# Performance work log

Hardware: AMD Instinct MI355X
Metric: run time of the kernel (lower is better)

The kernel has to match this reference:

```python
import jax, jax.numpy as jnp
import numpy as np

N, E = 4096, 131072
D_IN, D_H, H, D_HEAD, D_OUT, L = 768, 256, 4, 64, 128, 2


def setup_inputs() -> dict:
    key = jax.random.key(0)
    ks = jax.random.split(key, 8)
    x = jax.random.normal(ks[0], (N, D_IN), dtype=jnp.float32)
    edge_index = jax.random.randint(ks[1], (2, E), 0, N, dtype=jnp.int64)
    Win = jax.random.normal(ks[2], (D_IN, D_H), dtype=jnp.float32) * 0.02
    bin_ = jnp.zeros((D_H,), dtype=jnp.float32)
    # per-layer, per-head projection weights [L, H, D_H, D_HEAD]
    Wg = jax.random.normal(ks[3], (L, H, D_H, D_HEAD), dtype=jnp.float32) * 0.05
    # per-layer, per-head attention vectors a: [L, H, 2*D_HEAD]
    a = jax.random.normal(ks[4], (L, H, 2 * D_HEAD), dtype=jnp.float32) * 0.05
    Wout = jax.random.normal(ks[5], (D_H, D_OUT), dtype=jnp.float32) * 0.05
    bout = jnp.zeros((D_OUT,), dtype=jnp.float32)
    return {"x": x, "edge_index": edge_index, "Win": Win, "bin_": bin_,
            "Wg": Wg, "a": a, "Wout": Wout, "bout": bout}


def _gat_layer(h, Wl, al, row, col):
    # h: [N, D_H], Wl: [H, D_H, D_HEAD], al: [H, 2*D_HEAD]
    hh = jnp.einsum('ni,hio->hno', h, Wl)          # [H, N, D_HEAD]
    a_src, a_dst = al[:, :D_HEAD], al[:, D_HEAD:]
    s_src = jnp.einsum('hno,ho->hn', hh, a_src)    # [H, N]
    s_dst = jnp.einsum('hno,ho->hn', hh, a_dst)    # [H, N]
    e = jax.nn.leaky_relu(s_src[:, row] + s_dst[:, col], negative_slope=0.2)  # [H, E]
    # dense scatter exactly as the torch module: zeros then assign at (row, col)
    att = jnp.zeros((H, N, N), dtype=h.dtype).at[:, row, col].set(e)
    att = jax.nn.softmax(att, axis=-1)             # dense row softmax (zeros included)
    hp = jnp.einsum('hnm,hmo->hno', att, hh)       # [H, N, D_HEAD]
    return jnp.transpose(hp, (1, 0, 2)).reshape(N, H * D_HEAD)


def reference(x, edge_index, Win, bin_, Wg, a, Wout, bout):
    row, col = edge_index[0], edge_index[1]
    h = jax.nn.relu(x @ Win + bin_)                # input_proj + relu (dropout = eval identity)
    for l in range(L):
        h = jax.nn.relu(_gat_layer(h, Wg[l], a[l], row, col))
    node_embeddings = h @ Wout + bout              # [N, D_OUT]
    return node_embeddings
```

## Files before the change

### kernel.cpp

```cpp
#include <hip/hip_runtime.h>
#include <hip/hip_bf16.h>

#define NNODES 4096
#define NEDGES 131072
#define D_IN   768
#define D_H    256
#define NHEAD  4
#define D_HEAD 64
#define D_OUT  128
#define DEGCAP 192
#define S_SCALE 1048576.0f

typedef __attribute__((ext_vector_type(4))) float f32x4;
typedef __attribute__((ext_vector_type(8))) short bf16x8;
typedef __attribute__((ext_vector_type(8))) unsigned short u16x8;

static __device__ __forceinline__ unsigned short f2bf(float f) {
    __hip_bfloat16 h = __float2bfloat16(f);
    return *reinterpret_cast<unsigned short*>(&h);
}
static __device__ __forceinline__ float bf2f(unsigned short u) {
    return __uint_as_float((unsigned)u << 16);
}

#define OFF_XB     (0u)
#define OFF_H0     (6u<<20)
#define OFF_H1     (8u<<20)
#define OFF_HH     (10u<<20)
#define OFF_SINT   (12u<<20)
#define OFF_SSRC   (OFF_SINT + 4096u)
#define OFF_SDST   (OFF_SSRC + 65536u)
#define OFF_WINT   (OFF_SDST + 65536u)
#define OFF_WGT    (OFF_WINT + 393216u)
#define OFF_WOUTT  (OFF_WGT + 262144u)
#define OFF_BM     (OFF_WOUTT + 65536u)

__global__ __launch_bounds__(256) void k_init(
    const float* __restrict__ Win, const float* __restrict__ Wg,
    const float* __restrict__ Wout, const float* __restrict__ x,
    unsigned short* __restrict__ WinT, unsigned short* __restrict__ WgT,
    unsigned short* __restrict__ WoutT, unsigned short* __restrict__ xb,
    uint4* __restrict__ bm4, unsigned long long* __restrict__ Sint)
{
    __shared__ float tile[32][33];
    const int tid = threadIdx.x, bid = blockIdx.x;
    bm4[bid*256 + tid] = make_uint4(0u,0u,0u,0u);
    if (bid == 0) { Sint[tid] = 0ull; Sint[256 + tid] = 0ull; }

    {
        const float4* x4 = (const float4*)x;
        ushort4* xb4 = (ushort4*)xb;
        for (int i = bid*256 + tid; i < (NNODES*D_IN)/4; i += 512*256) {
            float4 v = x4[i];
            ushort4 o;
            o.x = f2bf(v.x); o.y = f2bf(v.y); o.z = f2bf(v.z); o.w = f2bf(v.w);
            xb4[i] = o;
        }
    }

    if (bid < 352) {
        const float* src; unsigned short* dst; int R, Cc, tr, tc;
        if (bid < 192)      { src = Win;  dst = WinT;  R = 768; Cc = 256; tr = bid >> 3; tc = bid & 7; }
        else if (bid < 320) { int t = bid - 192; int m = t >> 4, s = t & 15;
                              src = Wg + (size_t)m*16384; dst = WgT + (size_t)m*16384;
                              R = 256; Cc = 64; tr = s >> 1; tc = s & 1; }
        else                { int t = bid - 320; src = Wout; dst = WoutT;
                              R = 256; Cc = 128; tr = t >> 2; tc = t & 3; }
        int ci = tid & 31, rq = tid >> 5;
        #pragma unroll
        for (int rr = rq; rr < 32; rr += 8)
            tile[rr][ci] = src[(size_t)(tr*32+rr)*Cc + tc*32 + ci];
        __syncthreads();
        int ri = tid & 31, cq = tid >> 5;
        #pragma unroll
        for (int cc = cq; cc < 32; cc += 8)
            dst[(size_t)(tc*32+cc)*R + tr*32 + ri] = f2bf(tile[ri][cc]);
    }
}

__global__ void edge_bitmap(const int* __restrict__ ei, unsigned* __restrict__ bm)
{
    __shared__ int is64_sh;
    int tid = threadIdx.x;
    if (tid < 64) {
        int v = ei[2*tid + 1];
        unsigned long long ball = __ballot(v == 0);
        if (tid == 0) is64_sh = (ball == ~0ull) ? 1 : 0;
    }
    __syncthreads();
    int is64 = is64_sh;
    int k = blockIdx.x*256 + tid;
    if (k >= NEDGES) return;
    int r = is64 ? ei[2*k]            : ei[k];
    int c = is64 ? ei[2*NEDGES + 2*k] : ei[NEDGES + k];
    r &= (NNODES-1); c &= (NNODES-1);
    atomicOr(&bm[(size_t)r*128 + (c>>5)], 1u << (c & 31));
}

__global__ __launch_bounds__(256) void gemm_mfma(
    const unsigned short* __restrict__ A, const unsigned short* __restrict__ BT,
    const float* __restrict__ bias, float* __restrict__ Cf,
    unsigned short* __restrict__ Cb,
    int N, int K, int relu,
    const float* __restrict__ a_l, float* __restrict__ ssrc,
    float* __restrict__ sdst, unsigned long long* __restrict__ Sint)
{
    __shared__ unsigned short As[32][72];
    __shared__ unsigned short Bs[64][72];
    __shared__ float sredS[4][32], sredD[4][32];
    const int tid = threadIdx.x;
    const int bx = blockIdx.x, by = blockIdx.y;
    const int wc = tid >> 6;
    const int lane = tid & 63;
    const int g = lane >> 4, c = lane & 15;
    const int ar = tid >> 3, ak = (tid & 7) * 8;
    const int bc = tid >> 2, bk = (tid & 3) * 16;
    f32x4 acc0 = {0.f,0.f,0.f,0.f}, acc1 = {0.f,0.f,0.f,0.f};
    const unsigned short* Arow = A + (size_t)(by*32 + ar)*K;
    const unsigned short* Brow = BT + (size_t)(bx*64 + bc)*K;

    for (int k0 = 0; k0 < K; k0 += 64) {
        u16x8 avv = *(const u16x8*)&Arow[k0 + ak];
        u16x8 bv0 = *(const u16x8*)&Brow[k0 + bk];
        u16x8 bv1 = *(const u16x8*)&Brow[k0 + bk + 8];
        *(u16x8*)&As[ar][ak]     = avv;
        *(u16x8*)&Bs[bc][bk]     = bv0;
        *(u16x8*)&Bs[bc][bk + 8] = bv1;
        __syncthreads();
        bf16x8 b0  = *(bf16x8*)&Bs[wc*16 + c][g*8];
        bf16x8 b1  = *(bf16x8*)&Bs[wc*16 + c][32 + g*8];
        bf16x8 a00 = *(bf16x8*)&As[c][g*8];
        bf16x8 a01 = *(bf16x8*)&As[c][32 + g*8];
        bf16x8 a10 = *(bf16x8*)&As[16 + c][g*8];
        bf16x8 a11 = *(bf16x8*)&As[16 + c][32 + g*8];
        acc0 = __builtin_amdgcn_mfma_f32_16x16x32_bf16(a00, b0, acc0, 0, 0, 0);
        acc0 = __builtin_amdgcn_mfma_f32_16x16x32_bf16(a01, b1, acc0, 0, 0, 0);
        acc1 = __builtin_amdgcn_mfma_f32_16x16x32_bf16(a10, b0, acc1, 0, 0, 0);
        acc1 = __builtin_amdgcn_mfma_f32_16x16x32_bf16(a11, b1, acc1, 0, 0, 0);
        __syncthreads();
    }

    const int col = bx*64 + wc*16 + c;
    float bb = bias ? bias[col] : 0.f;
    #pragma unroll
    for (int t = 0; t < 2; ++t) {
        f32x4 av = t ? acc1 : acc0;
        #pragma unroll
        for (int i = 0; i < 4; ++i) {
            int r = by*32 + t*16 + g*4 + i;
            float v = av[i] + bb;
            if (relu) v = fmaxf(v, 0.f);
            if (Cb) Cb[(size_t)r*N + col] = f2bf(v);
            else    Cf[(size_t)r*N + col] = v;
        }
    }

    if (a_l) {
        int h = bx;
        float as = a_l[h*128 + wc*16 + c];
        float ad = a_l[h*128 + 64 + wc*16 + c];
        float ps[8], pd[8], cs = 0.f;
        #pragma unroll
        for (int t = 0; t < 2; ++t) {
            f32x4 av = t ? acc1 : acc0;
            #pragma unroll
            for (int i = 0; i < 4; ++i) {
                ps[t*4+i] = av[i] * as;
                pd[t*4+i] = av[i] * ad;
                cs += av[i];
            }
        }
        #pragma unroll
        for (int off = 1; off < 16; off <<= 1) {
            #pragma unroll
            for (int j = 0; j < 8; ++j) {
                ps[j] += __shfl_xor(ps[j], off);
                pd[j] += __shfl_xor(pd[j], off);
            }
        }
        if (c == 0) {
            #pragma unroll
            for (int t = 0; t < 2; ++t)
                #pragma unroll
                for (int i = 0; i < 4; ++i) {
                    sredS[wc][t*16 + g*4 + i] = ps[t*4+i];
                    sredD[wc][t*16 + g*4 + i] = pd[t*4+i];
                }
        }
        cs += __shfl_xor(cs, 16);
        cs += __shfl_xor(cs, 32);
        if (g == 0) {
            long long q = (long long)llrintf(cs * S_SCALE);
            atomicAdd(&Sint[col], (unsigned long long)q);
        }
        __syncthreads();
        if (tid < 32) {
            float s1 = sredS[0][tid] + sredS[1][tid] + sredS[2][tid] + sredS[3][tid];
            float s2 = sredD[0][tid] + sredD[1][tid] + sredD[2][tid] + sredD[3][tid];
            int r = by*32 + tid;
            ssrc[r*4 + h] = s1;
            sdst[r*4 + h] = s2;
        }
    }
}

__global__ __launch_bounds__(256) void aggregate_kernel(
    const unsigned* __restrict__ bm,
    const float* __restrict__ ssrc, const float* __restrict__ sdst,
    const unsigned short* __restrict__ hh,
    const unsigned long long* __restrict__ Sint,
    unsigned short* __restrict__ hout)
{
    __shared__ int   csr_lds[DEGCAP];
    __shared__ float w_lds[4*DEGCAP];
    __shared__ int   cnt_sh;
    int n = blockIdx.x;
    int tid = threadIdx.x;
    int h = tid >> 6, o = tid & 63;
    const unsigned* brow = bm + (size_t)n*128;
    float Sv = (float)(long long)Sint[h*64 + o] * (1.0f / S_SCALE);

    if (tid < 64) {
        unsigned wA = brow[2*tid], wB = brow[2*tid + 1];
        int cpc = __popc(wA) + __popc(wB);
        int pre = cpc;
        #pragma unroll
        for (int off = 1; off < 64; off <<= 1) {
            int v = __shfl_up(pre, off);
            if (tid >= off) pre += v;
        }
        int excl = pre - cpc;
        int total = __shfl(pre, 63);
        if (total <= DEGCAP) {
            int pos = excl, base = tid*64;
            unsigned w = wA;
            while (w) { int b = __builtin_ctz(w); csr_lds[pos++] = base + b; w &= w-1; }
            w = wB; base += 32;
            while (w) { int b = __builtin_ctz(w); csr_lds[pos++] = base + b; w &= w-1; }
        }
        if (tid == 0) cnt_sh = total;
    }
    __syncthreads();
    int cnt = cnt_sh;
    float ss = ssrc[n*4 + h];

    if (cnt <= DEGCAP) {
        float mx = 0.f;
        for (int i = o; i < cnt; i += 64) {
            int m = csr_lds[i];
            float e = ss + sdst[m*4 + h];
            e = (e >= 0.f) ? e : 0.2f*e;
            mx = fmaxf(mx, e);
        }
        #pragma unroll
        for (int off = 32; off; off >>= 1) mx = fmaxf(mx, __shfl_xor(mx, off));
        float M = mx;
        float base = expf(-M);

        float zp = 0.f;
        for (int i = o; i < cnt; i += 64) {
            int m = csr_lds[i];
            float e = ss + sdst[m*4 + h];
            e = (e >= 0.f) ? e : 0.2f*e;
            float w = expf(e - M) - base;
            w_lds[h*DEGCAP + i] = w;
            zp += w;
        }
        #pragma unroll
        for (int off = 32; off; off >>= 1) zp += __shfl_xor(zp, off);

        float acc = 0.f;
        int i = 0;
        for (; i + 8 <= cnt; i += 8) {
            int   mm[8]; float wq[8]; float vq[8];
            #pragma unroll
            for (int j = 0; j < 8; ++j) {
                mm[j] = csr_lds[i+j];
                wq[j] = w_lds[h*DEGCAP + i + j];
            }
            #pragma unroll
            for (int j = 0; j < 8; ++j)
                vq[j] = bf2f(hh[(size_t)mm[j]*256 + h*64 + o]);
            #pragma unroll
            for (int j = 0; j < 8; ++j)
                acc += wq[j] * vq[j];
        }
        for (; i < cnt; ++i)
            acc += w_lds[h*DEGCAP+i] * bf2f(hh[(size_t)csr_lds[i]*256 + h*64 + o]);

        float Z  = zp + (float)NNODES * base;
        float hp = (acc + base * Sv) / Z;
        hout[(size_t)n*256 + h*64 + o] = f2bf(fmaxf(hp, 0.f));
    } else {
        float mx = 0.f;
        for (int m = o; m < NNODES; m += 64) {
            if ((brow[m>>5] >> (m & 31)) & 1u) {
                float e = ss + sdst[m*4 + h];
                e = (e >= 0.f) ? e : 0.2f*e;
                mx = fmaxf(mx, e);
            }
        }
        #pragma unroll
        for (int off = 32; off; off >>= 1) mx = fmaxf(mx, __shfl_xor(mx, off));
        float M = mx;
        float base = expf(-M);
        float zp = 0.f, acc = 0.f;
        for (int m = 0; m < NNODES; ++m) {
            if ((brow[m>>5] >> (m & 31)) & 1u) {
                float e = ss + sdst[m*4 + h];
                e = (e >= 0.f) ? e : 0.2f*e;
                float w = expf(e - M) - base;
                zp += w;
                acc += w * bf2f(hh[(size_t)m*256 + h*64 + o]);
            }
        }
        float Z  = zp + (float)NNODES * base;
        float hp = (acc + base * Sv) / Z;
        hout[(size_t)n*256 + h*64 + o] = f2bf(fmaxf(hp, 0.f));
    }
}

static int find_size(const int* sz, int n, int want, int fallback)
{
    for (int i = 0; i < n; ++i) if (sz[i] == want) return i;
    return fallback;
}

extern "C" void kernel_launch(void* const* d_in, const int* in_sizes, int n_in,
                              void* d_out, int out_size, void* d_ws, size_t ws_size,
                              hipStream_t stream)
{
    int ix   = find_size(in_sizes, n_in, NNODES*D_IN, 0);
    int ie   = find_size(in_sizes, n_in, 2*NEDGES, 1);
    int iwin = find_size(in_sizes, n_in, D_IN*D_H, 2);
    int ibin = find_size(in_sizes, n_in, D_H, 3);
    int iwg  = find_size(in_sizes, n_in, 2*NHEAD*D_H*D_HEAD, 4);
    int ia   = find_size(in_sizes, n_in, 2*NHEAD*2*D_HEAD, 5);
    int iwo  = find_size(in_sizes, n_in, D_H*D_OUT, 6);
    int ibo  = find_size(in_sizes, n_in, D_OUT, 7);

    const float* x    = (const float*)d_in[ix];
    const int*   ei   = (const int*)d_in[ie];
    const float* Win  = (const float*)d_in[iwin];
    const float* bin_ = (const float*)d_in[ibin];
    const float* Wg   = (const float*)d_in[iwg];
    const float* a    = (const float*)d_in[ia];
    const float* Wout = (const float*)d_in[iwo];
    const float* bout = (const float*)d_in[ibo];
    float* out = (float*)d_out;

    char* ws = (char*)d_ws;
    unsigned short*     xb    = (unsigned short*)(ws + OFF_XB);
    unsigned short*     h0    = (unsigned short*)(ws + OFF_H0);
    unsigned short*     h1    = (unsigned short*)(ws + OFF_H1);
    unsigned short*     hh    = (unsigned short*)(ws + OFF_HH);
    unsigned long long* Sint  = (unsigned long long*)(ws + OFF_SINT);
    float*              ssrc  = (float*)(ws + OFF_SSRC);
    float*              sdst  = (float*)(ws + OFF_SDST);
    unsigned short*     WinT  = (unsigned short*)(ws + OFF_WINT);
    unsigned short*     WgT   = (unsigned short*)(ws + OFF_WGT);
    unsigned short*     WoutT = (unsigned short*)(ws + OFF_WOUTT);
    unsigned*           bm    = (unsigned*)(ws + OFF_BM);

    k_init<<<512, 256, 0, stream>>>(Win, Wg, Wout, x, WinT, WgT, WoutT, xb,
                                    (uint4*)bm, Sint);
    edge_bitmap<<<NEDGES/256, 256, 0, stream>>>(ei, bm);

    {
        dim3 g(D_H/64, NNODES/32);
        gemm_mfma<<<g, 256, 0, stream>>>(xb, WinT, bin_, nullptr, h0,
                                         D_H, D_IN, 1,
                                         nullptr, nullptr, nullptr, nullptr);
    }

    unsigned short* hin = h0;
    unsigned short* hcur = h1;
    for (int l = 0; l < 2; ++l) {
        dim3 g2(D_H/64, NNODES/32);
        gemm_mfma<<<g2, 256, 0, stream>>>(hin, WgT + (size_t)l*NHEAD*D_HEAD*D_H,
                                          nullptr, nullptr, hh,
                                          D_H, D_H, 0,
                                          a + (size_t)l*NHEAD*128, ssrc, sdst,
                                          Sint + (size_t)l*256);
        aggregate_kernel<<<NNODES, 256, 0, stream>>>(bm, ssrc, sdst, hh,
                                                     Sint + (size_t)l*256, hcur);
        unsigned short* t = hin; hin = hcur; hcur = t;
    }

    {
        dim3 g(D_OUT/64, NNODES/32);
        gemm_mfma<<<g, 256, 0, stream>>>(hin, WoutT, bout, out, nullptr,
                                         D_OUT, D_H, 0,
                                         nullptr, nullptr, nullptr, nullptr);
    }
}
```

Before: 79.66 us.

## Fuse edge bitmap build into input GEMM and compute CSR per head wave

The separate edge_bitmap kernel is removed. Its atomicOr work is appended to the tail of the input-projection GEMM, which is launched as a 1D grid of 512 blocks, with block indices remapped so neighbouring blocks spread across XCDs. In the aggregate kernel every wave now builds the CSR list redundantly, which removes the shared count variable and a block barrier. It also caches the leaky-relu scores in LDS instead of recomputing them for the softmax pass. This saves one launch and a sync, at the cost of redundant bitmap scans and concurrent LDS writes of identical values by four waves.

Result: no change. 79.72 us, median of 2 (+0.1%).

```diff
diff --git a/kernel.cpp b/kernel.cpp
--- a/kernel.cpp
+++ b/kernel.cpp
@@ -78,38 +78,28 @@
     }
 }
 
-__global__ void edge_bitmap(const int* __restrict__ ei, unsigned* __restrict__ bm)
-{
-    __shared__ int is64_sh;
-    int tid = threadIdx.x;
-    if (tid < 64) {
-        int v = ei[2*tid + 1];
-        unsigned long long ball = __ballot(v == 0);
-        if (tid == 0) is64_sh = (ball == ~0ull) ? 1 : 0;
-    }
-    __syncthreads();
-    int is64 = is64_sh;
-    int k = blockIdx.x*256 + tid;
-    if (k >= NEDGES) return;
-    int r = is64 ? ei[2*k]            : ei[k];
-    int c = is64 ? ei[2*NEDGES + 2*k] : ei[NEDGES + k];
-    r &= (NNODES-1); c &= (NNODES-1);
-    atomicOr(&bm[(size_t)r*128 + (c>>5)], 1u << (c & 31));
-}
-
 __global__ __launch_bounds__(256) void gemm_mfma(
     const unsigned short* __restrict__ A, const unsigned short* __restrict__ BT,
     const float* __restrict__ bias, float* __restrict__ Cf,
     unsigned short* __restrict__ Cb,
     int N, int K, int relu,
     const float* __restrict__ a_l, float* __restrict__ ssrc,
-    float* __restrict__ sdst, unsigned long long* __restrict__ Sint)
+    float* __restrict__ sdst, unsigned long long* __restrict__ Sint,
+    const int* __restrict__ ei, unsigned* __restrict__ bm)
 {
     __shared__ unsigned short As[32][72];
     __shared__ unsigned short Bs[64][72];
     __shared__ float sredS[4][32], sredD[4][32];
     const int tid = threadIdx.x;
-    const int bx = blockIdx.x, by = blockIdx.y;
+    int bx, by;
+    if (ei) {
+        int bid = blockIdx.x;
+        int xcd = bid & 7, q = bid >> 3;
+        bx = q & 3;
+        by = (q >> 2)*8 + xcd;
+    } else {
+        bx = blockIdx.x; by = blockIdx.y;
+    }
     const int wc = tid >> 6;
     const int lane = tid & 63;
     const int g = lane >> 4, c = lane & 15;
@@ -202,6 +192,23 @@
             sdst[r*4 + h] = s2;
         }
     }
+
+    if (ei) {
+        __shared__ int flag;
+        int bid = blockIdx.x;
+        if (tid < 64) {
+            int v = ei[2*tid + 1];
+            unsigned long long ball = __ballot(v == 0);
+            if (tid == 0) flag = (ball == ~0ull) ? 1 : 0;
+        }
+        __syncthreads();
+        int is64 = flag;
+        int k = bid*256 + tid;
+        int r  = is64 ? ei[2*k]            : ei[k];
+        int cc = is64 ? ei[2*NEDGES + 2*k] : ei[NEDGES + k];
+        r &= (NNODES-1); cc &= (NNODES-1);
+        atomicOr(&bm[(size_t)r*128 + (cc>>5)], 1u << (cc & 31));
+    }
 }
 
 __global__ __launch_bounds__(256) void aggregate_kernel(
@@ -213,35 +220,29 @@
 {
     __shared__ int   csr_lds[DEGCAP];
     __shared__ float w_lds[4*DEGCAP];
-    __shared__ int   cnt_sh;
     int n = blockIdx.x;
     int tid = threadIdx.x;
     int h = tid >> 6, o = tid & 63;
     const unsigned* brow = bm + (size_t)n*128;
     float Sv = (float)(long long)Sint[h*64 + o] * (1.0f / S_SCALE);
 
-    if (tid < 64) {
-        unsigned wA = brow[2*tid], wB = brow[2*tid + 1];
-        int cpc = __popc(wA) + __popc(wB);
-        int pre = cpc;
-        #pragma unroll
-        for (int off = 1; off < 64; off <<= 1) {
-            int v = __shfl_up(pre, off);
-            if (tid >= off) pre += v;
-        }
-        int excl = pre - cpc;
-        int total = __shfl(pre, 63);
-        if (total <= DEGCAP) {
-            int pos = excl, base = tid*64;
-            unsigned w = wA;
-            while (w) { int b = __builtin_ctz(w); csr_lds[pos++] = base + b; w &= w-1; }
-            w = wB; base += 32;
-            while (w) { int b = __builtin_ctz(w); csr_lds[pos++] = base + b; w &= w-1; }
-        }
-        if (tid == 0) cnt_sh = total;
-    }
-    __syncthreads();
-    int cnt = cnt_sh;
+    unsigned wA = brow[2*o], wB = brow[2*o + 1];
+    int cpc = __popc(wA) + __popc(wB);
+    int pre = cpc;
+    #pragma unroll
+    for (int off = 1; off < 64; off <<= 1) {
+        int v = __shfl_up(pre, off);
+        if (o >= off) pre += v;
+    }
+    int excl = pre - cpc;
+    int cnt = __shfl(pre, 63);
+    if (cnt <= DEGCAP) {
+        int pos = excl, base = o*64;
+        unsigned w = wA;
+        while (w) { int b = __builtin_ctz(w); csr_lds[pos++] = base + b; w &= w-1; }
+        w = wB; base += 32;
+        while (w) { int b = __builtin_ctz(w); csr_lds[pos++] = base + b; w &= w-1; }
+    }
     float ss = ssrc[n*4 + h];
 
     if (cnt <= DEGCAP) {
@@ -250,6 +251,7 @@
             int m = csr_lds[i];
             float e = ss + sdst[m*4 + h];
             e = (e >= 0.f) ? e : 0.2f*e;
+            w_lds[h*DEGCAP + i] = e;
             mx = fmaxf(mx, e);
         }
         #pragma unroll
@@ -259,10 +261,7 @@
 
         float zp = 0.f;
         for (int i = o; i < cnt; i += 64) {
-            int m = csr_lds[i];
-            float e = ss + sdst[m*4 + h];
-            e = (e >= 0.f) ? e : 0.2f*e;
-            float w = expf(e - M) - base;
+            float w = expf(w_lds[h*DEGCAP + i] - M) - base;
             w_lds[h*DEGCAP + i] = w;
             zp += w;
         }
@@ -364,14 +363,11 @@
 
     k_init<<<512, 256, 0, stream>>>(Win, Wg, Wout, x, WinT, WgT, WoutT, xb,
                                     (uint4*)bm, Sint);
-    edge_bitmap<<<NEDGES/256, 256, 0, stream>>>(ei, bm);
-
-    {
-        dim3 g(D_H/64, NNODES/32);
-        gemm_mfma<<<g, 256, 0, stream>>>(xb, WinT, bin_, nullptr, h0,
-                                         D_H, D_IN, 1,
-                                         nullptr, nullptr, nullptr, nullptr);
-    }
+
+    gemm_mfma<<<512, 256, 0, stream>>>(xb, WinT, bin_, nullptr, h0,
+                                       D_H, D_IN, 1,
+                                       nullptr, nullptr, nullptr, nullptr,
+                                       ei, bm);
 
     unsigned short* hin = h0;
     unsigned short* hcur = h1;
@@ -381,7 +377,8 @@
                                           nullptr, nullptr, hh,
                                           D_H, D_H, 0,
                                           a + (size_t)l*NHEAD*128, ssrc, sdst,
-                                          Sint + (size_t)l*256);
+                                          Sint + (size_t)l*256,
+                                          nullptr, nullptr);
         aggregate_kernel<<<NNODES, 256, 0, stream>>>(bm, ssrc, sdst, hh,
                                                      Sint + (size_t)l*256, hcur);
         unsigned short* t = hin; hin = hcur; hcur = t;
@@ -391,6 +388,7 @@
         dim3 g(D_OUT/64, NNODES/32);
         gemm_mfma<<<g, 256, 0, stream>>>(hin, WoutT, bout, out, nullptr,
                                          D_OUT, D_H, 0,
-                                         nullptr, nullptr, nullptr, nullptr);
-    }
-}
+                                         nullptr, nullptr, nullptr, nullptr,
+                                         nullptr, nullptr);
+    }
+}
```
